# Optimization experiments

Measured on AMD Instinct MI355X. Metric: run time of the kernel, lower is better.

The kernel has to match this reference:

```python
import jax, jax.numpy as jnp
import numpy as np
from jax import lax

GN_GROUPS = 8
GN_EPS = 1e-5
K_BITS = 8
DELTA = 0.05
EPS = 1e-8


def setup_inputs() -> dict:
    key = jax.random.key(0)
    k1, k2 = jax.random.split(key)
    B, Cin, H, W = 32, 256, 56, 56
    Cout, KS = 256, 3
    x = jax.random.normal(k1, (B, Cin, H, W), dtype=jnp.float32)
    # kaiming_normal_(nonlinearity='relu'): std = sqrt(2 / fan_in)
    fan_in = Cin * KS * KS
    weight_fp = jax.random.normal(k2, (Cout, Cin, KS, KS), dtype=jnp.float32) * np.sqrt(2.0 / fan_in)
    gamma = jnp.ones((Cin,), dtype=jnp.float32)
    beta = jnp.zeros((Cin,), dtype=jnp.float32)
    a = jnp.asarray(6.0, dtype=jnp.float32)  # PACT learnable clip
    bias = jnp.zeros((Cout,), dtype=jnp.float32)
    return {"x": x, "gamma": gamma, "beta": beta, "a": a, "weight_fp": weight_fp, "bias": bias}


def _group_norm(x, gamma, beta):
    B, C, H, W = x.shape
    xg = x.reshape(B, GN_GROUPS, -1)
    mu = xg.mean(axis=-1, keepdims=True)
    var = xg.var(axis=-1, keepdims=True)  # biased, matches torch GroupNorm
    xn = ((xg - mu) * lax.rsqrt(var + GN_EPS)).reshape(B, C, H, W)
    return xn * gamma[:, None, None] + beta[:, None, None]


def _pact_quant(x, a):
    a_c = jnp.maximum(a, 0.0) + EPS
    S = (2.0 ** K_BITS - 1.0) / a_c
    y = jnp.clip(x, 0.0, a_c)
    # straight-through round
    return y + lax.stop_gradient(jnp.round(y * S) / S - y)


def _ternary_weight(w_r):
    oc = w_r.shape[0]
    wv = w_r.reshape(oc, -1)
    wa = jnp.abs(wv)
    t = DELTA * wa.mean(axis=1, keepdims=True)
    m = (wa > t).astype(wv.dtype)
    alpha = (wa * m).sum(axis=1, keepdims=True) / (m.sum(axis=1, keepdims=True) + EPS)
    wq = (alpha * jnp.sign(wv) * m).reshape(w_r.shape)
    # STE gradient factor: m + 0.5*(1 - m)
    g = lax.stop_gradient((0.5 + 0.5 * m).reshape(w_r.shape))
    return g * w_r + lax.stop_gradient(wq - g * w_r)


def reference(x, gamma, beta, a, weight_fp, bias):
    h = _group_norm(x, gamma, beta)
    h = jnp.maximum(h, 0.0) ** 2          # ReLU^2
    h = _pact_quant(h, a)                  # PACT k-bit uniform quant
    w = _ternary_weight(weight_fp)         # ternary {-alpha, 0, +alpha}
    out = lax.conv_general_dilated(
        h, w, window_strides=(1, 1), padding=[(1, 1), (1, 1)],
        dimension_numbers=("NCHW", "OIHW", "NCHW"))
    return out + bias[:, None, None]
```

## Files before the change

kernel.cpp:

```cpp
#include <hip/hip_runtime.h>
#include <hip/hip_bf16.h>

#define B_    32
#define C_    256
#define H_    56
#define W_    56
#define HW_   3136
#define P_    58
#define G_    8
#define COUT_ 256
#define KTOT_ 2304

typedef float f32x4 __attribute__((ext_vector_type(4)));
typedef int   i32x4 __attribute__((ext_vector_type(4)));

__global__ __launch_bounds__(256)
void gn_partial_kernel(const float* __restrict__ x, float2* __restrict__ partial) {
    int blk = blockIdx.x;
    const float4* base = (const float4*)(x + (size_t)blk * 12544);
    float s1 = 0.f, s2 = 0.f;
    for (int i = threadIdx.x; i < 3136; i += 256) {
        float4 v = base[i];
        s1 += v.x + v.y + v.z + v.w;
        s2 += v.x * v.x + v.y * v.y + v.z * v.z + v.w * v.w;
    }
    #pragma unroll
    for (int off = 32; off; off >>= 1) {
        s1 += __shfl_down(s1, off, 64);
        s2 += __shfl_down(s2, off, 64);
    }
    __shared__ float ra[4], rb[4];
    int lane = threadIdx.x & 63, wv = threadIdx.x >> 6;
    if (!lane) { ra[wv] = s1; rb[wv] = s2; }
    __syncthreads();
    if (threadIdx.x == 0) {
        float2 p;
        p.x = ra[0] + ra[1] + ra[2] + ra[3];
        p.y = rb[0] + rb[1] + rb[2] + rb[3];
        partial[blk] = p;
    }
}

__global__ __launch_bounds__(256)
void act_kernel(const float* __restrict__ x, const float* __restrict__ gamma,
                const float* __restrict__ beta, const float* __restrict__ a_ptr,
                const float2* __restrict__ partial, char* __restrict__ q) {
    int by = blockIdx.x;
    int b = by / P_;
    int y = by - b * P_;
    char* qrow = q + (size_t)by * P_ * C_;
    const int PADV = 0x80808080;
    if (y == 0 || y == P_ - 1) {
        int4 pv = {PADV, PADV, PADV, PADV};
        for (int i = threadIdx.x; i < (P_ * C_) / 16; i += 256)
            ((int4*)qrow)[i] = pv;
        return;
    }
    int t = threadIdx.x;
    if (t < 64)            ((int*)qrow)[t] = PADV;
    else if (t < 128)      ((int*)(qrow + (P_ - 1) * C_))[t - 64] = PADV;

    __shared__ float4 xs[256 * 16];
    const float* xb2 = x + (size_t)b * C_ * HW_ + (y - 1) * W_;
    #pragma unroll
    for (int k = 0; k < 14; ++k) {
        int idx = t + k * 256;
        int c   = idx / 14;
        int jj  = idx - c * 14;
        int key = (c >> 2) & 7;
        xs[c * 16 + (jj ^ key)] = *(const float4*)(xb2 + (size_t)c * HW_ + jj * 4);
    }
    __syncthreads();

    float a_c = fmaxf(a_ptr[0], 0.f) + 1e-8f;
    float S   = 255.f / a_c;

    int c4 = t & 63;
    int wb = t >> 6;
    int g  = c4 >> 3;
    const float2* pp = partial + ((size_t)b * G_ + g) * 8;
    float s1 = 0.f, s2 = 0.f;
    #pragma unroll
    for (int p = 0; p < 8; ++p) { s1 += pp[p].x; s2 += pp[p].y; }
    float mu = s1 / 100352.f;
    float var = s2 / 100352.f - mu * mu;
    float rs = rsqrtf(var + 1e-5f);

    float ga[4], be[4];
    #pragma unroll
    for (int i = 0; i < 4; ++i) { ga[i] = gamma[4 * c4 + i]; be[i] = beta[4 * c4 + i]; }

    int rkey = c4 & 7;
    for (int j = wb; j < 14; j += 4) {
        float4 v[4];
        #pragma unroll
        for (int i = 0; i < 4; ++i)
            v[i] = xs[(4 * c4 + i) * 16 + (j ^ rkey)];
        int qv[4][4];
        #pragma unroll
        for (int i = 0; i < 4; ++i) {
            float f[4] = {v[i].x, v[i].y, v[i].z, v[i].w};
            #pragma unroll
            for (int s = 0; s < 4; ++s) {
                float yv = (f[s] - mu) * rs * ga[i] + be[i];
                float r  = fmaxf(yv, 0.f);
                float h2 = fminf(r * r, a_c);
                qv[i][s] = (int)rintf(h2 * S) - 128;
            }
        }
        #pragma unroll
        for (int s = 0; s < 4; ++s) {
            int packed = (qv[0][s] & 255) | ((qv[1][s] & 255) << 8) |
                         ((qv[2][s] & 255) << 16) | (qv[3][s] << 24);
            *(int*)(qrow + (j * 4 + s + 1) * C_ + 4 * c4) = packed;
        }
    }
}

__global__ __launch_bounds__(256)
void wq_kernel(const float* __restrict__ wfp, char* __restrict__ wt,
               float* __restrict__ alphas, float* __restrict__ tsum) {
    int oc = blockIdx.x;
    int t  = threadIdx.x;
    const float* wr = wfp + (size_t)oc * KTOT_;
    float wl[9];
    float s = 0.f;
    #pragma unroll
    for (int j = 0; j < 9; ++j) { wl[j] = wr[t + j * 256]; s += fabsf(wl[j]); }

    __shared__ float red[4];
    int lane = t & 63, wv = t >> 6;
    #pragma unroll
    for (int off = 32; off; off >>= 1) s += __shfl_down(s, off, 64);
    if (!lane) red[wv] = s;
    __syncthreads();
    float thr = 0.05f * ((red[0] + red[1] + red[2] + red[3]) / (float)KTOT_);
    __syncthreads();

    float sm = 0.f, cnt = 0.f, ts = 0.f;
    #pragma unroll
    for (int j = 0; j < 9; ++j) {
        float aw = fabsf(wl[j]);
        if (aw > thr) {
            sm += aw; cnt += 1.f;
            ts += (wl[j] > 0.f) ? 1.f : -1.f;
        }
    }
    #pragma unroll
    for (int off = 32; off; off >>= 1) {
        sm  += __shfl_down(sm, off, 64);
        cnt += __shfl_down(cnt, off, 64);
        ts  += __shfl_down(ts, off, 64);
    }
    __shared__ float redc[4], redt[4];
    if (!lane) { red[wv] = sm; redc[wv] = cnt; redt[wv] = ts; }
    __syncthreads();
    if (t == 0) {
        float alpha = (red[0] + red[1] + red[2] + red[3]) /
                      (redc[0] + redc[1] + redc[2] + redc[3] + 1e-8f);
        alphas[oc] = alpha;
        tsum[oc] = redt[0] + redt[1] + redt[2] + redt[3];
    }
    #pragma unroll
    for (int j = 0; j < 9; ++j) {
        int i  = t + j * 256;
        int ic = i / 9;
        int tap = i - ic * 9;
        float w = wl[j];
        char tern = (fabsf(w) > thr) ? (w > 0.f ? (char)1 : (char)-1) : (char)0;
        wt[((size_t)tap * 256 + oc) * 256 + ic] = tern;
    }
}

__global__ __launch_bounds__(512)
void conv_gemm_kernel(const char* __restrict__ q, const char* __restrict__ wt,
                      const float* __restrict__ alphas, const float* __restrict__ bias,
                      const float* __restrict__ tsum, const float* __restrict__ a_ptr,
                      float* __restrict__ out) {
    int bid = blockIdx.x;
    int mt = (bid & 7) * 98 + (bid >> 3);
    int tid = threadIdx.x;
    int lane = tid & 63;
    int wv = tid >> 6;
    int wm = wv & 1, wn = wv >> 1;
    int quad = lane >> 4, lrow = lane & 15;

    __shared__ char As[128 * 128];
    __shared__ char Bs[256 * 128];

    int kswz = (((tid & 7) ^ ((tid >> 3) & 7)) << 4);
    int sb[2], wb[4];
    #pragma unroll
    for (int r = 0; r < 2; ++r) {
        int ml = r * 64 + (tid >> 3);
        int m = mt * 128 + ml;
        int b = m / HW_;
        int rem = m - b * HW_;
        int hh = rem / W_;
        int ww = rem - hh * W_;
        sb[r] = ((b * P_ + hh + 1) * P_ + (ww + 1)) * C_ + kswz;
    }
    #pragma unroll
    for (int r = 0; r < 4; ++r) {
        int oc = r * 64 + (tid >> 3);
        wb[r] = oc * C_ + kswz;
    }

    i32x4 acc[4][4];
    #pragma unroll
    for (int i = 0; i < 4; ++i)
        #pragma unroll
        for (int j = 0; j < 4; ++j) { acc[i][j][0]=0; acc[i][j][1]=0; acc[i][j][2]=0; acc[i][j][3]=0; }

    int arow = wm * 64 + lrow;
    int brow = wn * 64 + lrow;
    int rsw = lrow & 7;

    for (int kk = 0; kk < 18; ++kk) {
        int tap = kk >> 1;
        int ic0 = (kk & 1) << 7;
        int dh = tap / 3 - 1;
        int dw = tap - (tap / 3) * 3 - 1;
        int aoff = (dh * P_ + dw) * C_ + ic0;
        const char* gb = wt + (size_t)tap * (256 * 256) + ic0;
        #pragma unroll
        for (int r = 0; r < 2; ++r) {
            __builtin_amdgcn_global_load_lds(
                (const __attribute__((address_space(1))) void*)(q + sb[r] + aoff),
                (__attribute__((address_space(3))) void*)(&As[r * 8192 + tid * 16]),
                16, 0, 0);
        }
        #pragma unroll
        for (int r = 0; r < 4; ++r) {
            __builtin_amdgcn_global_load_lds(
                (const __attribute__((address_space(1))) void*)(gb + wb[r]),
                (__attribute__((address_space(3))) void*)(&Bs[r * 8192 + tid * 16]),
                16, 0, 0);
        }
        __syncthreads();
        #pragma unroll
        for (int ks = 0; ks < 2; ++ks) {
            int cb = (ks * 4 + quad) ^ rsw;
            i32x4 af[4], bf[4];
            #pragma unroll
            for (int mi = 0; mi < 4; ++mi)
                af[mi] = *(const i32x4*)&As[(arow + mi * 16) * 128 + cb * 16];
            #pragma unroll
            for (int ni = 0; ni < 4; ++ni)
                bf[ni] = *(const i32x4*)&Bs[(brow + ni * 16) * 128 + cb * 16];
            #pragma unroll
            for (int mi = 0; mi < 4; ++mi)
                #pragma unroll
                for (int ni = 0; ni < 4; ++ni)
                    acc[mi][ni] = __builtin_amdgcn_mfma_i32_16x16x64_i8(
                        af[mi], bf[ni], acc[mi][ni], 0, 0, 0);
        }
        __syncthreads();
    }

    float a_c = fmaxf(a_ptr[0], 0.f) + 1e-8f;
    float qs  = a_c * (1.f / 255.f);
    #pragma unroll
    for (int ni = 0; ni < 4; ++ni) {
        int n = wn * 64 + ni * 16 + lrow;
        float sc = alphas[n] * qs;
        float bn = bias[n];
        float corr = 128.f * tsum[n];
        #pragma unroll
        for (int mi = 0; mi < 4; ++mi) {
            int mbase = mt * 128 + wm * 64 + mi * 16 + quad * 4;
            int b = mbase / HW_;
            size_t off = (size_t)b * (C_ * HW_) + (size_t)n * HW_ + (mbase - b * HW_);
            f32x4 v;
            #pragma unroll
            for (int r = 0; r < 4; ++r)
                v[r] = ((float)acc[mi][ni][r] + corr) * sc + bn;
            *(f32x4*)(out + off) = v;
        }
    }
}

extern "C" void kernel_launch(void* const* d_in, const int* in_sizes, int n_in,
                              void* d_out, int out_size, void* d_ws, size_t ws_size,
                              hipStream_t stream) {
    const float* x     = (const float*)d_in[0];
    const float* gamma = (const float*)d_in[1];
    const float* beta  = (const float*)d_in[2];
    const float* a     = (const float*)d_in[3];
    const float* wfp   = (const float*)d_in[4];
    const float* bias  = (const float*)d_in[5];
    float* out = (float*)d_out;

    char* ws = (char*)d_ws;
    char*   qbuf    = ws;
    char*   wtb     = ws + 27557888;
    float*  alphas  = (float*)(ws + 27557888 + 589824);
    float*  tsum    = alphas + 256;
    float2* partial = (float2*)(tsum + 256);

    gn_partial_kernel<<<2048, 256, 0, stream>>>(x, partial);
    wq_kernel<<<COUT_, 256, 0, stream>>>(wfp, wtb, alphas, tsum);
    act_kernel<<<B_ * P_, 256, 0, stream>>>(x, gamma, beta, a, partial, qbuf);
    conv_gemm_kernel<<<784, 512, 0, stream>>>(qbuf, wtb, alphas, bias, tsum, a, out);
}
```

Measured before the change: 279.2 us.

## Triple-buffer LDS in int8 conv GEMM with async global-to-LDS prefetch

Replaces the single-buffered load/sync/compute loop with a three-stage LDS ring (48KB per stage), issuing global_load_lds for stage k+2 while computing stage k, synchronized with partial vmcnt waits and raw barriers. It also raises wave priority around the MFMA block. The aim is to hide global memory latency behind matrix math. In exchange LDS use per block grows to 144KB, which limits blocks per CU to one, and the hand-written vmcnt counts must exactly match the six outstanding loads per stage.

```diff
diff --git a/kernel.cpp b/kernel.cpp
--- a/kernel.cpp
+++ b/kernel.cpp
@@ -185,8 +185,10 @@
     int wm = wv & 1, wn = wv >> 1;
     int quad = lane >> 4, lrow = lane & 15;
 
-    __shared__ char As[128 * 128];
-    __shared__ char Bs[256 * 128];
+    __shared__ char lds[3 * 49152];
+    char* const bufA = &lds[0];
+    char* const bufB = &lds[49152];
+    char* const bufC = &lds[98304];
 
     int kswz = (((tid & 7) ^ ((tid >> 3) & 7)) << 4);
     int sb[2], wb[4];
@@ -216,47 +218,82 @@
     int brow = wn * 64 + lrow;
     int rsw = lrow & 7;
 
-    for (int kk = 0; kk < 18; ++kk) {
+    auto stage = [&](int kk, char* base) {
         int tap = kk >> 1;
         int ic0 = (kk & 1) << 7;
         int dh = tap / 3 - 1;
         int dw = tap - (tap / 3) * 3 - 1;
         int aoff = (dh * P_ + dw) * C_ + ic0;
-        const char* gb = wt + (size_t)tap * (256 * 256) + ic0;
         #pragma unroll
         for (int r = 0; r < 2; ++r) {
             __builtin_amdgcn_global_load_lds(
                 (const __attribute__((address_space(1))) void*)(q + sb[r] + aoff),
-                (__attribute__((address_space(3))) void*)(&As[r * 8192 + tid * 16]),
+                (__attribute__((address_space(3))) void*)(base + r * 8192 + tid * 16),
                 16, 0, 0);
         }
+        const char* gb = wt + (size_t)tap * (256 * 256) + ic0;
         #pragma unroll
         for (int r = 0; r < 4; ++r) {
             __builtin_amdgcn_global_load_lds(
                 (const __attribute__((address_space(1))) void*)(gb + wb[r]),
-                (__attribute__((address_space(3))) void*)(&Bs[r * 8192 + tid * 16]),
+                (__attribute__((address_space(3))) void*)(base + 16384 + r * 8192 + tid * 16),
                 16, 0, 0);
         }
-        __syncthreads();
+    };
+
+    auto compute = [&](const char* base) {
+        const char* Asb = base;
+        const char* Bsb = base + 16384;
         #pragma unroll
         for (int ks = 0; ks < 2; ++ks) {
             int cb = (ks * 4 + quad) ^ rsw;
             i32x4 af[4], bf[4];
             #pragma unroll
             for (int mi = 0; mi < 4; ++mi)
-                af[mi] = *(const i32x4*)&As[(arow + mi * 16) * 128 + cb * 16];
+                af[mi] = *(const i32x4*)&Asb[(arow + mi * 16) * 128 + cb * 16];
             #pragma unroll
             for (int ni = 0; ni < 4; ++ni)
-                bf[ni] = *(const i32x4*)&Bs[(brow + ni * 16) * 128 + cb * 16];
+                bf[ni] = *(const i32x4*)&Bsb[(brow + ni * 16) * 128 + cb * 16];
+            __builtin_amdgcn_s_setprio(1);
             #pragma unroll
             for (int mi = 0; mi < 4; ++mi)
                 #pragma unroll
                 for (int ni = 0; ni < 4; ++ni)
                     acc[mi][ni] = __builtin_amdgcn_mfma_i32_16x16x64_i8(
                         af[mi], bf[ni], acc[mi][ni], 0, 0, 0);
-        }
-        __syncthreads();
-    }
+            __builtin_amdgcn_s_setprio(0);
+        }
+    };
+
+    stage(0, bufA);
+    stage(1, bufB);
+
+    #pragma unroll 1
+    for (int t6 = 0; t6 < 5; ++t6) {
+        int t = t6 * 3;
+        asm volatile("s_waitcnt vmcnt(6)" ::: "memory");
+        __builtin_amdgcn_s_barrier();
+        stage(t + 2, bufC);
+        compute(bufA);
+        asm volatile("s_waitcnt vmcnt(6)" ::: "memory");
+        __builtin_amdgcn_s_barrier();
+        stage(t + 3, bufA);
+        compute(bufB);
+        asm volatile("s_waitcnt vmcnt(6)" ::: "memory");
+        __builtin_amdgcn_s_barrier();
+        stage(t + 4, bufB);
+        compute(bufC);
+    }
+    asm volatile("s_waitcnt vmcnt(6)" ::: "memory");
+    __builtin_amdgcn_s_barrier();
+    stage(17, bufC);
+    compute(bufA);
+    asm volatile("s_waitcnt vmcnt(6)" ::: "memory");
+    __builtin_amdgcn_s_barrier();
+    compute(bufB);
+    asm volatile("s_waitcnt vmcnt(0)" ::: "memory");
+    __builtin_amdgcn_s_barrier();
+    compute(bufC);
 
     float a_c = fmaxf(a_ptr[0], 0.f) + 1e-8f;
     float qs  = a_c * (1.f / 255.f);
```

Measured after the change: 291.0 us. 1.04x slower.

## Load GEMM fragments directly from global memory, dropping LDS staging

Applied to the files above, without the earlier changes.

The int8 conv GEMM no longer stages A and B tiles through shared memory with barriers. Each wave now reads its MFMA fragments straight from global memory, relying on cache for reuse. The output-channel dimension is split across two blocks, using 256-thread blocks, twice the grid, and occupancy hints. This removes LDS traffic and synchronization, but every wave re-reads overlapping data from L1/L2 and gives up the cross-wave sharing that LDS provided.

```diff
diff --git a/kernel.cpp b/kernel.cpp
--- a/kernel.cpp
+++ b/kernel.cpp
@@ -172,39 +172,35 @@
     }
 }
 
-__global__ __launch_bounds__(512)
+__global__ __launch_bounds__(256, 3)
 void conv_gemm_kernel(const char* __restrict__ q, const char* __restrict__ wt,
                       const float* __restrict__ alphas, const float* __restrict__ bias,
                       const float* __restrict__ tsum, const float* __restrict__ a_ptr,
                       float* __restrict__ out) {
     int bid = blockIdx.x;
-    int mt = (bid & 7) * 98 + (bid >> 3);
+    int virt = (bid & 7) * 196 + (bid >> 3);
+    int mt = virt >> 1;
+    int nh = virt & 1;
     int tid = threadIdx.x;
     int lane = tid & 63;
     int wv = tid >> 6;
     int wm = wv & 1, wn = wv >> 1;
     int quad = lane >> 4, lrow = lane & 15;
 
-    __shared__ char As[128 * 128];
-    __shared__ char Bs[256 * 128];
-
-    int kswz = (((tid & 7) ^ ((tid >> 3) & 7)) << 4);
-    int sb[2], wb[4];
-    #pragma unroll
-    for (int r = 0; r < 2; ++r) {
-        int ml = r * 64 + (tid >> 3);
-        int m = mt * 128 + ml;
+    int aoff[4];
+    #pragma unroll
+    for (int mi = 0; mi < 4; ++mi) {
+        int m = mt * 128 + wm * 64 + lrow + mi * 16;
         int b = m / HW_;
         int rem = m - b * HW_;
         int hh = rem / W_;
         int ww = rem - hh * W_;
-        sb[r] = ((b * P_ + hh + 1) * P_ + (ww + 1)) * C_ + kswz;
-    }
-    #pragma unroll
-    for (int r = 0; r < 4; ++r) {
-        int oc = r * 64 + (tid >> 3);
-        wb[r] = oc * C_ + kswz;
-    }
+        aoff[mi] = ((b * P_ + hh + 1) * P_ + (ww + 1)) * C_ + quad * 16;
+    }
+    int boff[4];
+    #pragma unroll
+    for (int ni = 0; ni < 4; ++ni)
+        boff[ni] = (nh * 128 + wn * 64 + ni * 16 + lrow) * 256 + quad * 16;
 
     i32x4 acc[4][4];
     #pragma unroll
@@ -212,42 +208,23 @@
         #pragma unroll
         for (int j = 0; j < 4; ++j) { acc[i][j][0]=0; acc[i][j][1]=0; acc[i][j][2]=0; acc[i][j][3]=0; }
 
-    int arow = wm * 64 + lrow;
-    int brow = wn * 64 + lrow;
-    int rsw = lrow & 7;
-
+    #pragma unroll
     for (int kk = 0; kk < 18; ++kk) {
-        int tap = kk >> 1;
-        int ic0 = (kk & 1) << 7;
-        int dh = tap / 3 - 1;
-        int dw = tap - (tap / 3) * 3 - 1;
-        int aoff = (dh * P_ + dw) * C_ + ic0;
-        const char* gb = wt + (size_t)tap * (256 * 256) + ic0;
-        #pragma unroll
-        for (int r = 0; r < 2; ++r) {
-            __builtin_amdgcn_global_load_lds(
-                (const __attribute__((address_space(1))) void*)(q + sb[r] + aoff),
-                (__attribute__((address_space(3))) void*)(&As[r * 8192 + tid * 16]),
-                16, 0, 0);
-        }
-        #pragma unroll
-        for (int r = 0; r < 4; ++r) {
-            __builtin_amdgcn_global_load_lds(
-                (const __attribute__((address_space(1))) void*)(gb + wb[r]),
-                (__attribute__((address_space(3))) void*)(&Bs[r * 8192 + tid * 16]),
-                16, 0, 0);
-        }
-        __syncthreads();
+        const int tap = kk >> 1;
+        const int ic0 = (kk & 1) << 7;
+        const int dh  = tap / 3 - 1;
+        const int dw  = tap - (tap / 3) * 3 - 1;
+        const char* qk = q  + ((dh * P_ + dw) * C_ + ic0);
+        const char* wk = wt + tap * 65536 + ic0;
         #pragma unroll
         for (int ks = 0; ks < 2; ++ks) {
-            int cb = (ks * 4 + quad) ^ rsw;
             i32x4 af[4], bf[4];
             #pragma unroll
             for (int mi = 0; mi < 4; ++mi)
-                af[mi] = *(const i32x4*)&As[(arow + mi * 16) * 128 + cb * 16];
+                af[mi] = *(const i32x4*)(qk + aoff[mi] + ks * 64);
             #pragma unroll
             for (int ni = 0; ni < 4; ++ni)
-                bf[ni] = *(const i32x4*)&Bs[(brow + ni * 16) * 128 + cb * 16];
+                bf[ni] = *(const i32x4*)(wk + boff[ni] + ks * 64);
             #pragma unroll
             for (int mi = 0; mi < 4; ++mi)
                 #pragma unroll
@@ -255,14 +232,13 @@
                     acc[mi][ni] = __builtin_amdgcn_mfma_i32_16x16x64_i8(
                         af[mi], bf[ni], acc[mi][ni], 0, 0, 0);
         }
-        __syncthreads();
     }
 
     float a_c = fmaxf(a_ptr[0], 0.f) + 1e-8f;
     float qs  = a_c * (1.f / 255.f);
     #pragma unroll
     for (int ni = 0; ni < 4; ++ni) {
-        int n = wn * 64 + ni * 16 + lrow;
+        int n = nh * 128 + wn * 64 + ni * 16 + lrow;
         float sc = alphas[n] * qs;
         float bn = bias[n];
         float corr = 128.f * tsum[n];
@@ -301,5 +277,5 @@
     gn_partial_kernel<<<2048, 256, 0, stream>>>(x, partial);
     wq_kernel<<<COUT_, 256, 0, stream>>>(wfp, wtb, alphas, tsum);
     act_kernel<<<B_ * P_, 256, 0, stream>>>(x, gamma, beta, a, partial, qbuf);
-    conv_gemm_kernel<<<784, 512, 0, stream>>>(qbuf, wtb, alphas, bias, tsum, a, out);
-}
+    conv_gemm_kernel<<<1568, 256, 0, stream>>>(qbuf, wtb, alphas, bias, tsum, a, out);
+}
```

Measured after the change: 436.5 us. 1.56x slower.
